# Kernel tuning notes

Measured on AMD Instinct MI355X. Metric: run time of the kernel, lower is better.

The kernel has to match this reference:

```python
import jax, jax.numpy as jnp
import numpy as np

NUM_NODES = 100000
NUM_REL_P1 = 238  # num_relations + 1 (extra column for self-connection relation id -1)
B = 32768
S = 16
D_IN = 256
D_OUT = 256


def setup_inputs() -> dict:
    key = jax.random.key(0)
    k1, k2, k3, k4, k5 = jax.random.split(key, 5)
    neighbors = jax.random.randint(k1, (B, S), 0, NUM_NODES)          # sampled neighbor node ids
    relations = jax.random.randint(k2, (B, S), 0, NUM_REL_P1)          # sampled relation ids
    features = jax.random.normal(k3, (NUM_NODES, D_IN), dtype=jnp.float32)
    weight = jax.random.normal(k4, (D_OUT, D_IN), dtype=jnp.float32) * (1.0 / np.sqrt(D_IN))
    relation_weight = jax.random.normal(k5, (D_OUT, NUM_REL_P1), dtype=jnp.float32) * 0.05
    return {"neighbors": neighbors, "relations": relations, "features": features,
            "weight": weight, "relation_weight": relation_weight}


def reference(neighbors, relations, features, weight, relation_weight):
    # gather sampled neighbor embeddings: [B, S, D_in]
    neighbor_emb = features[neighbors]
    # mean-aggregate over the sample dim: [B, D_in]
    agg_neighbors = neighbor_emb.mean(axis=1)
    # linear transform: [B, D_in] @ [D_in, D_out] -> [B, D_out]
    agg_neighbors = agg_neighbors @ weight.T
    # gather + mean relation embeddings: [B, S, D_out] -> [B, D_out]
    agg_relations = relation_weight.T[relations].mean(axis=1)
    return jax.nn.relu(agg_neighbors + agg_relations)
```

## Files before the change

### kernel.cpp

```cpp
#include <hip/hip_runtime.h>

#define B_ROWS  32768
#define S_SAMP  16
#define NRELS   238
#define DIM     256
#define N_NODES 100000
#define NF4     ((N_NODES * DIM) / 4)
#define CONV_BLOCKS (NF4 / 256)

typedef __attribute__((ext_vector_type(8))) short  short8;
typedef __attribute__((ext_vector_type(4))) float  f32x4;

static __device__ __forceinline__ unsigned short f2bf(float f) {
    unsigned int u = __float_as_uint(f);
    u += 0x7FFFu + ((u >> 16) & 1u);
    return (unsigned short)(u >> 16);
}
static __device__ __forceinline__ float bf2f(unsigned short u) {
    return __uint_as_float(((unsigned int)u) << 16);
}

__global__ __launch_bounds__(256) void prep_kernel(const float* __restrict__ F,
                                                   const float* __restrict__ W,
                                                   const float* __restrict__ RW,
                                                   unsigned short* __restrict__ Fb,
                                                   unsigned short* __restrict__ Wb,
                                                   unsigned short* __restrict__ RWTb) {
    if (blockIdx.x < CONV_BLOCKS) {
        int i = blockIdx.x * 256 + threadIdx.x;
        float4 v = ((const float4*)F)[i];
        ushort4 p;
        p.x = f2bf(v.x); p.y = f2bf(v.y); p.z = f2bf(v.z); p.w = f2bf(v.w);
        ((ushort4*)Fb)[i] = p;
    } else {
        int i = (blockIdx.x - CONV_BLOCKS) * 256 + threadIdx.x;
        if (i < DIM * DIM) Wb[i] = f2bf(W[i]);
        if (i < NRELS * DIM) {
            int r = i >> 8;
            int d = i & 255;
            RWTb[i] = f2bf(RW[d * NRELS + r]);
        }
    }
}

__global__ __launch_bounds__(256) void fused_kernel(const int* __restrict__ nbr,
                                                    const int* __restrict__ rels,
                                                    const unsigned short* __restrict__ Fb,
                                                    const unsigned short* __restrict__ RWTb,
                                                    const unsigned short* __restrict__ Wb,
                                                    float* __restrict__ out) {
    __shared__ unsigned short As[32][264];
    __shared__ unsigned short Rs[32][264];
    const int tid  = threadIdx.x;
    const int lane = tid & 63;
    const int wid  = __builtin_amdgcn_readfirstlane(tid >> 6);
    const int col0 = lane & 15;
    const int quad = lane >> 4;
    const int r0g  = blockIdx.x * 32;

    const float sc = 1.0f / 16.0f;
    for (int i = 0; i < 8; ++i) {
        const int row_l = wid * 8 + i;
        const int row_g = r0g + row_l;
        const int2* nb2 = (const int2*)(nbr  + row_g * S_SAMP);
        const int2* rl2 = (const int2*)(rels + row_g * S_SAMP);
        float a0 = 0.f, a1 = 0.f, a2 = 0.f, a3 = 0.f;
        float b0 = 0.f, b1 = 0.f, b2 = 0.f, b3 = 0.f;
#pragma unroll
        for (int t = 0; t < 8; ++t) {
            int2 nn = nb2[t];
            int2 rr = rl2[t];
            ushort4 f0 = *(const ushort4*)(Fb   + (size_t)nn.x * DIM + lane * 4);
            ushort4 g0 = *(const ushort4*)(RWTb + (size_t)rr.x * DIM + lane * 4);
            ushort4 f1 = *(const ushort4*)(Fb   + (size_t)nn.y * DIM + lane * 4);
            ushort4 g1 = *(const ushort4*)(RWTb + (size_t)rr.y * DIM + lane * 4);
            a0 += bf2f(f0.x) + bf2f(f1.x);
            a1 += bf2f(f0.y) + bf2f(f1.y);
            a2 += bf2f(f0.z) + bf2f(f1.z);
            a3 += bf2f(f0.w) + bf2f(f1.w);
            b0 += bf2f(g0.x) + bf2f(g1.x);
            b1 += bf2f(g0.y) + bf2f(g1.y);
            b2 += bf2f(g0.z) + bf2f(g1.z);
            b3 += bf2f(g0.w) + bf2f(g1.w);
        }
        ushort4 pa, pr;
        pa.x = f2bf(a0 * sc); pa.y = f2bf(a1 * sc); pa.z = f2bf(a2 * sc); pa.w = f2bf(a3 * sc);
        pr.x = f2bf(b0 * sc); pr.y = f2bf(b1 * sc); pr.z = f2bf(b2 * sc); pr.w = f2bf(b3 * sc);
        *(ushort4*)&As[row_l][lane * 4] = pa;
        *(ushort4*)&Rs[row_l][lane * 4] = pr;
    }

    short8 Breg[4][8];
#pragma unroll
    for (int j = 0; j < 4; ++j) {
#pragma unroll
        for (int kk = 0; kk < 8; ++kk) {
            int n = wid * 4 + j;
            Breg[j][kk] = *(const short8*)(Wb + (size_t)(n * 16 + col0) * DIM
                                              + kk * 32 + quad * 8);
        }
    }
    __syncthreads();

    f32x4 acc[2][4];
#pragma unroll
    for (int mt = 0; mt < 2; ++mt)
#pragma unroll
        for (int j = 0; j < 4; ++j) acc[mt][j] = (f32x4){0.f, 0.f, 0.f, 0.f};

#pragma unroll
    for (int mt = 0; mt < 2; ++mt) {
        const int mrow = mt * 16 + col0;
#pragma unroll
        for (int kk = 0; kk < 8; ++kk) {
            short8 af = *(const short8*)&As[mrow][kk * 32 + quad * 8];
#pragma unroll
            for (int j = 0; j < 4; ++j)
                acc[mt][j] = __builtin_amdgcn_mfma_f32_16x16x32_bf16(af, Breg[j][kk], acc[mt][j], 0, 0, 0);
        }
    }

#pragma unroll
    for (int mt = 0; mt < 2; ++mt) {
#pragma unroll
        for (int j = 0; j < 4; ++j) {
            const int col = (wid * 4 + j) * 16 + col0;
#pragma unroll
            for (int i2 = 0; i2 < 4; ++i2) {
                const int r_l = mt * 16 + quad * 4 + i2;
                float v = acc[mt][j][i2] + bf2f(Rs[r_l][col]);
                out[(size_t)(r0g + r_l) * DIM + col] = v > 0.f ? v : 0.f;
            }
        }
    }
}

extern "C" void kernel_launch(void* const* d_in, const int* in_sizes, int n_in,
                              void* d_out, int out_size, void* d_ws, size_t ws_size,
                              hipStream_t stream) {
    const int*   neighbors = (const int*)d_in[0];
    const int*   relations = (const int*)d_in[1];
    const float* features  = (const float*)d_in[2];
    const float* weight    = (const float*)d_in[3];
    const float* relw      = (const float*)d_in[4];
    float* out = (float*)d_out;

    char* ws = (char*)d_ws;
    unsigned short* Wb   = (unsigned short*)ws;
    unsigned short* RWTb = (unsigned short*)(ws + 131072);
    unsigned short* Fb   = (unsigned short*)(ws + 253952);

    prep_kernel<<<CONV_BLOCKS + 256, 256, 0, stream>>>(features, weight, relw, Fb, Wb, RWTb);
    fused_kernel<<<B_ROWS / 32, 256, 0, stream>>>(neighbors, relations, Fb, RWTb, Wb, out);
}
```

Baseline: 240.9 us.

## Widen gather loads to 16 bytes, split halves across F/R, halve B-register footprint

Each wavefront half now gathers one of the two samples per step with 16-byte loads covering the full row, and a cross-half shuffle combines the partial sums so one half writes the feature mean and the other the relation mean. The weight fragments are loaded in two K-halves, halving the register array. Launch bounds request 4 blocks per SM to raise occupancy for the latency-bound gather. The cost is an extra shuffle per element and a second round of weight loads in the middle of the MFMA sequence.

```diff
diff --git a/kernel.cpp b/kernel.cpp
--- a/kernel.cpp
+++ b/kernel.cpp
@@ -9,6 +9,7 @@
 #define CONV_BLOCKS (NF4 / 256)
 
 typedef __attribute__((ext_vector_type(8))) short  short8;
+typedef __attribute__((ext_vector_type(8))) unsigned short ushort8;
 typedef __attribute__((ext_vector_type(4))) float  f32x4;
 
 static __device__ __forceinline__ unsigned short f2bf(float f) {
@@ -43,17 +44,19 @@
     }
 }
 
-__global__ __launch_bounds__(256) void fused_kernel(const int* __restrict__ nbr,
-                                                    const int* __restrict__ rels,
-                                                    const unsigned short* __restrict__ Fb,
-                                                    const unsigned short* __restrict__ RWTb,
-                                                    const unsigned short* __restrict__ Wb,
-                                                    float* __restrict__ out) {
+__global__ __launch_bounds__(256, 4) void fused_kernel(const int* __restrict__ nbr,
+                                                       const int* __restrict__ rels,
+                                                       const unsigned short* __restrict__ Fb,
+                                                       const unsigned short* __restrict__ RWTb,
+                                                       const unsigned short* __restrict__ Wb,
+                                                       float* __restrict__ out) {
     __shared__ unsigned short As[32][264];
     __shared__ unsigned short Rs[32][264];
     const int tid  = threadIdx.x;
     const int lane = tid & 63;
     const int wid  = __builtin_amdgcn_readfirstlane(tid >> 6);
+    const int half = lane >> 5;
+    const int li   = lane & 31;
     const int col0 = lane & 15;
     const int quad = lane >> 4;
     const int r0g  = blockIdx.x * 32;
@@ -64,42 +67,38 @@
         const int row_g = r0g + row_l;
         const int2* nb2 = (const int2*)(nbr  + row_g * S_SAMP);
         const int2* rl2 = (const int2*)(rels + row_g * S_SAMP);
-        float a0 = 0.f, a1 = 0.f, a2 = 0.f, a3 = 0.f;
-        float b0 = 0.f, b1 = 0.f, b2 = 0.f, b3 = 0.f;
+        float af[8] = {0.f, 0.f, 0.f, 0.f, 0.f, 0.f, 0.f, 0.f};
+        float ag[8] = {0.f, 0.f, 0.f, 0.f, 0.f, 0.f, 0.f, 0.f};
 #pragma unroll
         for (int t = 0; t < 8; ++t) {
             int2 nn = nb2[t];
             int2 rr = rl2[t];
-            ushort4 f0 = *(const ushort4*)(Fb   + (size_t)nn.x * DIM + lane * 4);
-            ushort4 g0 = *(const ushort4*)(RWTb + (size_t)rr.x * DIM + lane * 4);
-            ushort4 f1 = *(const ushort4*)(Fb   + (size_t)nn.y * DIM + lane * 4);
-            ushort4 g1 = *(const ushort4*)(RWTb + (size_t)rr.y * DIM + lane * 4);
-            a0 += bf2f(f0.x) + bf2f(f1.x);
-            a1 += bf2f(f0.y) + bf2f(f1.y);
-            a2 += bf2f(f0.z) + bf2f(f1.z);
-            a3 += bf2f(f0.w) + bf2f(f1.w);
-            b0 += bf2f(g0.x) + bf2f(g1.x);
-            b1 += bf2f(g0.y) + bf2f(g1.y);
-            b2 += bf2f(g0.z) + bf2f(g1.z);
-            b3 += bf2f(g0.w) + bf2f(g1.w);
+            int nid = half ? nn.y : nn.x;
+            int rid = half ? rr.y : rr.x;
+            ushort8 f = *(const ushort8*)(Fb   + (size_t)nid * DIM + li * 8);
+            ushort8 g = *(const ushort8*)(RWTb + (size_t)rid * DIM + li * 8);
+#pragma unroll
+            for (int j = 0; j < 8; ++j) { af[j] += bf2f(f[j]); ag[j] += bf2f(g[j]); }
         }
-        ushort4 pa, pr;
-        pa.x = f2bf(a0 * sc); pa.y = f2bf(a1 * sc); pa.z = f2bf(a2 * sc); pa.w = f2bf(a3 * sc);
-        pr.x = f2bf(b0 * sc); pr.y = f2bf(b1 * sc); pr.z = f2bf(b2 * sc); pr.w = f2bf(b3 * sc);
-        *(ushort4*)&As[row_l][lane * 4] = pa;
-        *(ushort4*)&Rs[row_l][lane * 4] = pr;
+        ushort8 pk;
+#pragma unroll
+        for (int j = 0; j < 8; ++j) {
+            float mine = half ? ag[j] : af[j];
+            float send = half ? af[j] : ag[j];
+            float full = mine + __shfl_xor(send, 32, 64);
+            pk[j] = f2bf(full * sc);
+        }
+        unsigned short* dst = half ? &Rs[row_l][li * 8] : &As[row_l][li * 8];
+        *(ushort8*)dst = pk;
     }
 
-    short8 Breg[4][8];
+    short8 Breg[4][4];
 #pragma unroll
-    for (int j = 0; j < 4; ++j) {
+    for (int j = 0; j < 4; ++j)
 #pragma unroll
-        for (int kk = 0; kk < 8; ++kk) {
-            int n = wid * 4 + j;
-            Breg[j][kk] = *(const short8*)(Wb + (size_t)(n * 16 + col0) * DIM
+        for (int kk = 0; kk < 4; ++kk)
+            Breg[j][kk] = *(const short8*)(Wb + (size_t)((wid * 4 + j) * 16 + col0) * DIM
                                               + kk * 32 + quad * 8);
-        }
-    }
     __syncthreads();
 
     f32x4 acc[2][4];
@@ -112,11 +111,28 @@
     for (int mt = 0; mt < 2; ++mt) {
         const int mrow = mt * 16 + col0;
 #pragma unroll
-        for (int kk = 0; kk < 8; ++kk) {
-            short8 af = *(const short8*)&As[mrow][kk * 32 + quad * 8];
+        for (int kk = 0; kk < 4; ++kk) {
+            short8 a = *(const short8*)&As[mrow][kk * 32 + quad * 8];
 #pragma unroll
             for (int j = 0; j < 4; ++j)
-                acc[mt][j] = __builtin_amdgcn_mfma_f32_16x16x32_bf16(af, Breg[j][kk], acc[mt][j], 0, 0, 0);
+                acc[mt][j] = __builtin_amdgcn_mfma_f32_16x16x32_bf16(a, Breg[j][kk], acc[mt][j], 0, 0, 0);
+        }
+    }
+#pragma unroll
+    for (int j = 0; j < 4; ++j)
+#pragma unroll
+        for (int kk = 0; kk < 4; ++kk)
+            Breg[j][kk] = *(const short8*)(Wb + (size_t)((wid * 4 + j) * 16 + col0) * DIM
+                                              + (kk + 4) * 32 + quad * 8);
+#pragma unroll
+    for (int mt = 0; mt < 2; ++mt) {
+        const int mrow = mt * 16 + col0;
+#pragma unroll
+        for (int kk = 0; kk < 4; ++kk) {
+            short8 a = *(const short8*)&As[mrow][(kk + 4) * 32 + quad * 8];
+#pragma unroll
+            for (int j = 0; j < 4; ++j)
+                acc[mt][j] = __builtin_amdgcn_mfma_f32_16x16x32_bf16(a, Breg[j][kk], acc[mt][j], 0, 0, 0);
         }
     }
 
```

Result: faster. 217.5 us (-9.7%).
